# Kernel optimization log

Measured on AMD Instinct MI355X. Metric: run time of the kernel, lower is better.

The kernel has to match this reference:

```python
import jax, jax.numpy as jnp
import numpy as np

HEAD_DIM = 256
NUM_HEADS = 8
NUM_KV = 1
MAX_WAVELENGTH = 10000.0


def _apply_rope(x, positions):
    # x: [B, S, N, H], positions: [B, S] int
    d = x.shape[-1]
    freq_exponents = (2.0 / d) * jnp.arange(d // 2, dtype=jnp.float32)
    timescale = MAX_WAVELENGTH ** freq_exponents  # [H/2]
    radians = positions[..., None].astype(jnp.float32) / timescale  # [B, S, H/2]
    radians = radians[..., None, :]  # [B, S, 1, H/2]
    sin, cos = jnp.sin(radians), jnp.cos(radians)
    first, second = jnp.split(x.astype(jnp.float32), 2, axis=-1)
    out = jnp.concatenate([first * cos - second * sin, second * cos + first * sin], axis=-1)
    return out.astype(x.dtype)


def setup_inputs() -> dict:
    key = jax.random.key(0)
    ks = jax.random.split(key, 8)
    B, S0, S1 = 4, 768, 256
    W0, W1 = 2048, 1024
    T = S0 + S1
    s = 0.02  # param init scale
    x0 = jax.random.normal(ks[0], (B, S0, W0), jnp.float32)
    x1 = jax.random.normal(ks[1], (B, S1, W1), jnp.float32)
    w_q0 = jax.random.normal(ks[2], (NUM_HEADS, W0, HEAD_DIM), jnp.float32) * s
    w_kv0 = jax.random.normal(ks[3], (2, NUM_KV, W0, HEAD_DIM), jnp.float32) * s
    w_out0 = jax.random.normal(ks[4], (NUM_HEADS, HEAD_DIM, W0), jnp.float32) * s
    w_q1 = jax.random.normal(ks[5], (NUM_HEADS, W1, HEAD_DIM), jnp.float32) * s
    w_kv1 = jax.random.normal(ks[6], (2, NUM_KV, W1, HEAD_DIM), jnp.float32) * s
    w_out1 = jax.random.normal(ks[7], (NUM_HEADS, HEAD_DIM, W1), jnp.float32) * s
    positions = jnp.broadcast_to(jnp.arange(T, dtype=jnp.int32), (B, T))
    attn_mask = jnp.broadcast_to(jnp.tril(jnp.ones((T, T), bool))[None, None], (B, 1, T, T))
    return {"x0": x0, "x1": x1, "w_q0": w_q0, "w_kv0": w_kv0, "w_out0": w_out0,
            "w_q1": w_q1, "w_kv1": w_kv1, "w_out1": w_out1,
            "positions": positions, "attn_mask": attn_mask}


def reference(x0, x1, w_q0, w_kv0, w_out0, w_q1, w_kv1, w_out1, positions, attn_mask):
    dtype = x0.dtype
    # GQA projections per stream (num_kv_heads != num_heads path)
    q0 = jnp.einsum('BTD,NDH->BTNH', x0, w_q0)
    k0, v0 = jnp.einsum('BSD,CKDH->CBSKH', x0, w_kv0)
    q1 = jnp.einsum('BTD,NDH->BTNH', x1, w_q1)
    k1, v1 = jnp.einsum('BSD,CKDH->CBSKH', x1, w_kv1)
    q = jnp.concatenate([q0, q1], axis=1)  # [B, T, N, H]
    k = jnp.concatenate([k0, k1], axis=1)  # [B, T, K, H]
    v = jnp.concatenate([v0, v1], axis=1)
    q = _apply_rope(q, positions) * (HEAD_DIM ** -0.5)
    k = _apply_rope(k, positions)
    B, T = q.shape[0], q.shape[1]
    G = NUM_HEADS // NUM_KV
    q = q.reshape(B, T, NUM_KV, G, HEAD_DIM)
    logits = jnp.einsum('BTKGH,BSKH->BKGTS', q, k, preferred_element_type=jnp.float32)
    big_neg = -2.3819763e38
    masked = jnp.where(attn_mask[:, :, None, :, :], logits, big_neg)
    probs = jax.nn.softmax(masked, axis=-1).astype(dtype)
    encoded = jnp.einsum('BKGTS,BSKH->BTKGH', probs, v).reshape(B, T, NUM_HEADS, HEAD_DIM)
    S0 = x0.shape[1]
    out0 = jnp.einsum('BTNH,NHD->BTD', encoded[:, :S0], w_out0)
    out1 = jnp.einsum('BTNH,NHD->BTD', encoded[:, S0:], w_out1)
    return (out0, out1, k, v)
```

## Files before the change

kernel.cpp:

```cpp
#include <hip/hip_runtime.h>
#include <hip/hip_bf16.h>

typedef __attribute__((ext_vector_type(8))) short bf16x8;
typedef __attribute__((ext_vector_type(4))) float f32x4;
typedef __attribute__((ext_vector_type(4))) unsigned short u16x4;
typedef unsigned short US;

__device__ __forceinline__ f32x4 mfma16(bf16x8 a, bf16x8 b, f32x4 c) {
  return __builtin_amdgcn_mfma_f32_16x16x32_bf16(a, b, c, 0, 0, 0);
}

__device__ __forceinline__ US f2bf(float f) {
  union { float f; unsigned u; } x; x.f = f;
  unsigned r = x.u + 0x7fffu + ((x.u >> 16) & 1u);
  return (US)(r >> 16);
}

__device__ __forceinline__ void gld16(const US* gp, US* lp) {
  __builtin_amdgcn_global_load_lds(
      (const __attribute__((address_space(1))) unsigned*)gp,
      (__attribute__((address_space(3))) unsigned*)lp, 16, 0, 0);
}

__device__ __forceinline__ int permq(int h) {
  return ((h >> 5) << 6) + (h & 15) + (((h >> 4) & 1) << 5);
}

__device__ __forceinline__ int map_row(int r, int mode) {
  if (mode == 1) { int b = r / 768; return b * 1024 + (r - b * 768); }
  if (mode == 2) { int b = r >> 8; return b * 1024 + 768 + (r & 255); }
  return r;
}

__global__ __launch_bounds__(256)
void k_sincos(const int* __restrict__ pos, float2* __restrict__ sct) {
  int idx = blockIdx.x * 256 + threadIdx.x;
  int bt = idx >> 7, j = idx & 127;
  float inv_ts = powf(10000.0f, -(float)j * (1.0f / 128.0f));
  float r = (float)pos[bt] * inv_ts;
  sct[idx] = make_float2(sinf(r), cosf(r));
}

__global__ __launch_bounds__(256)
void k_prep(const float* __restrict__ x0, const float* __restrict__ x1,
            US* __restrict__ x0b, US* __restrict__ x1b,
            const float* __restrict__ wq0, const float* __restrict__ wkv0,
            const float* __restrict__ wq1, const float* __restrict__ wkv1,
            const float* __restrict__ wo0, const float* __restrict__ wo1,
            US* __restrict__ btq0, US* __restrict__ btkv0,
            US* __restrict__ btq1, US* __restrict__ btkv1,
            US* __restrict__ bto0, US* __restrict__ bto1) {
  const int bid = blockIdx.x;
  const int tid = threadIdx.x;
  if (bid < 7168) {
    const float* src; US* dst; int i;
    if (bid < 6144) { src = x0; dst = x0b; i = bid * 256 + tid; }
    else            { src = x1; dst = x1b; i = (bid - 6144) * 256 + tid; }
    f32x4 v = *reinterpret_cast<const f32x4*>(src + (size_t)i * 4);
    u16x4 o;
    o[0] = f2bf(v[0]); o[1] = f2bf(v[1]); o[2] = f2bf(v[2]); o[3] = f2bf(v[3]);
    *reinterpret_cast<u16x4*>(dst + (size_t)i * 4) = o;
    return;
  }
  __shared__ float tile[32][33];
  const float* src; US* dst; int R, C, CX, local; long sbs, dbs; bool pq = false;
  if (bid < 11264)      { local = bid - 7168;  src = wq0;  dst = btq0;  R = 2048; C = 256;  CX = 8;  sbs = 2048L * 256; dbs = 256L * 2048; pq = true; }
  else if (bid < 12288) { local = bid - 11264; src = wkv0; dst = btkv0; R = 2048; C = 256;  CX = 8;  sbs = 2048L * 256; dbs = 256L * 2048; }
  else if (bid < 14336) { local = bid - 12288; src = wq1;  dst = btq1;  R = 1024; C = 256;  CX = 8;  sbs = 1024L * 256; dbs = 256L * 1024; pq = true; }
  else if (bid < 14848) { local = bid - 14336; src = wkv1; dst = btkv1; R = 1024; C = 256;  CX = 8;  sbs = 1024L * 256; dbs = 256L * 1024; }
  else if (bid < 18944) { local = bid - 14848; src = wo0;  dst = bto0;  R = 2048; C = 2048; CX = 64; sbs = 0; dbs = 0; }
  else                  { local = bid - 18944; src = wo1;  dst = bto1;  R = 2048; C = 1024; CX = 32; sbs = 0; dbs = 0; }
  const int RY = R >> 5;
  const int cx = local % CX;
  const int rest = local / CX;
  const int ry = rest % RY;
  const int z = rest / RY;
  const int c0 = cx * 32, r0 = ry * 32;
  const int tx = tid & 31, ty = tid >> 5;
  src += (long)z * sbs;
  dst += (long)z * dbs;
#pragma unroll
  for (int i = 0; i < 4; ++i)
    tile[ty + 8 * i][tx] = src[(size_t)(r0 + ty + 8 * i) * C + c0 + tx];
  __syncthreads();
#pragma unroll
  for (int i = 0; i < 4; ++i) {
    int h = c0 + ty + 8 * i;
    int ph = pq ? ((h < 128) ? permq(h) : permq(h - 128) + 16) : h;
    dst[(size_t)ph * R + r0 + tx] = f2bf(tile[tx][ty + 8 * i]);
  }
}

template <int CMAP>
__global__ __launch_bounds__(256, 2)
void k_gemm_qkv(const US* __restrict__ A, const US* __restrict__ BT,
                US* __restrict__ q_bf, float* __restrict__ Ckv,
                const float2* __restrict__ sct, int M, int K) {
  __shared__ __align__(16) US lA[2][128 * 32];
  __shared__ __align__(16) US lB[2][128 * 32];
  const int tid = threadIdx.x;
  const int lane = tid & 63;
  const int wid = tid >> 6;
  const int wm = wid >> 1, wn = wid & 1;
  const int m0 = blockIdx.y * 128, n0 = blockIdx.x * 128;
  const int g = lane >> 4, c = lane & 15;
  const int lrow = lane >> 2, lcol = (lane & 3) * 8;
  const size_t ga0 = (size_t)(m0 + wid * 16 + lrow) * K + lcol;
  const size_t ga1 = (size_t)(m0 + 64 + wid * 16 + lrow) * K + lcol;
  const size_t gb0 = (size_t)(n0 + wid * 16 + lrow) * K + lcol;
  const size_t gb1 = (size_t)(n0 + 64 + wid * 16 + lrow) * K + lcol;

  auto stage = [&](int bi, int k0) {
    gld16(A + ga0 + k0, &lA[bi][(wid * 16) * 32]);
    gld16(A + ga1 + k0, &lA[bi][(64 + wid * 16) * 32]);
    gld16(BT + gb0 + k0, &lB[bi][(wid * 16) * 32]);
    gld16(BT + gb1 + k0, &lB[bi][(64 + wid * 16) * 32]);
  };

  f32x4 acc[4][4];
#pragma unroll
  for (int i = 0; i < 4; ++i)
#pragma unroll
    for (int j = 0; j < 4; ++j) acc[i][j] = f32x4{0.f, 0.f, 0.f, 0.f};

  const int nt = K >> 5;
  stage(0, 0);
  __syncthreads();
  for (int t = 0; t < nt; ++t) {
    const int bi = t & 1;
    if (t + 1 < nt) stage(bi ^ 1, (t + 1) * 32);
    bf16x8 af[4], bfr[4];
#pragma unroll
    for (int i = 0; i < 4; ++i) {
      af[i] = *reinterpret_cast<const bf16x8*>(&lA[bi][(wm * 64 + i * 16 + c) * 32 + g * 8]);
      bfr[i] = *reinterpret_cast<const bf16x8*>(&lB[bi][(wn * 64 + i * 16 + c) * 32 + g * 8]);
    }
#pragma unroll
    for (int i = 0; i < 4; ++i)
#pragma unroll
      for (int j = 0; j < 4; ++j)
        acc[i][j] = mfma16(af[i], bfr[j], acc[i][j]);
    __syncthreads();
  }

  const int colb = n0 + wn * 64;
  if (colb < 2048) {
    const int n = colb >> 8;
    const int base64 = colb & 255;
    const int h0 = (base64 >> 6) * 32 + c;
    const float scale = 0.0625f;
#pragma unroll
    for (int i = 0; i < 4; ++i) {
#pragma unroll
      for (int r = 0; r < 4; ++r) {
        const int orow = map_row(m0 + wm * 64 + i * 16 + 4 * g + r, CMAP);
        const float2 sc0 = sct[orow * 128 + h0];
        const float2 sc1 = sct[orow * 128 + h0 + 16];
        US* qp = q_bf + ((size_t)orow * 8 + n) * 256 + base64 + c;
        const float q1 = acc[i][0][r], q2 = acc[i][1][r];
        const float q3 = acc[i][2][r], q4 = acc[i][3][r];
        qp[0]  = f2bf(scale * (q1 * sc0.y - q2 * sc0.x));
        qp[16] = f2bf(scale * (q2 * sc0.y + q1 * sc0.x));
        qp[32] = f2bf(scale * (q3 * sc1.y - q4 * sc1.x));
        qp[48] = f2bf(scale * (q4 * sc1.y + q3 * sc1.x));
      }
    }
  } else {
    const int nb = colb - 2048 + c;
#pragma unroll
    for (int i = 0; i < 4; ++i) {
#pragma unroll
      for (int r = 0; r < 4; ++r) {
        const int orow = map_row(m0 + wm * 64 + i * 16 + 4 * g + r, CMAP);
        float* cp = Ckv + (size_t)orow * 512 + nb;
#pragma unroll
        for (int j = 0; j < 4; ++j) cp[j * 16] = acc[i][j][r];
      }
    }
  }
}

__global__ __launch_bounds__(256, 2)
void k_gemm_out(const US* __restrict__ A, const US* __restrict__ BT0, const US* __restrict__ BT1,
                float* __restrict__ C0, float* __restrict__ C1) {
  const int m0 = blockIdx.y * 128, n0 = blockIdx.x * 128;
  const int s0 = m0 & 1023;
  const bool is0 = (s0 < 768);
  if (!is0 && n0 >= 1024) return;
  const US* __restrict__ BT = is0 ? BT0 : BT1;
  const int K = 2048;
  __shared__ __align__(16) US lA[2][128 * 32];
  __shared__ __align__(16) US lB[2][128 * 32];
  const int tid = threadIdx.x;
  const int lane = tid & 63;
  const int wid = tid >> 6;
  const int wm = wid >> 1, wn = wid & 1;
  const int g = lane >> 4, c = lane & 15;
  const int lrow = lane >> 2, lcol = (lane & 3) * 8;
  const size_t ga0 = (size_t)(m0 + wid * 16 + lrow) * K + lcol;
  const size_t ga1 = (size_t)(m0 + 64 + wid * 16 + lrow) * K + lcol;
  const size_t gb0 = (size_t)(n0 + wid * 16 + lrow) * K + lcol;
  const size_t gb1 = (size_t)(n0 + 64 + wid * 16 + lrow) * K + lcol;

  auto stage = [&](int bi, int k0) {
    gld16(A + ga0 + k0, &lA[bi][(wid * 16) * 32]);
    gld16(A + ga1 + k0, &lA[bi][(64 + wid * 16) * 32]);
    gld16(BT + gb0 + k0, &lB[bi][(wid * 16) * 32]);
    gld16(BT + gb1 + k0, &lB[bi][(64 + wid * 16) * 32]);
  };

  f32x4 acc[4][4];
#pragma unroll
  for (int i = 0; i < 4; ++i)
#pragma unroll
    for (int j = 0; j < 4; ++j) acc[i][j] = f32x4{0.f, 0.f, 0.f, 0.f};

  const int nt = K >> 5;
  stage(0, 0);
  __syncthreads();
  for (int t = 0; t < nt; ++t) {
    const int bi = t & 1;
    if (t + 1 < nt) stage(bi ^ 1, (t + 1) * 32);
    bf16x8 af[4], bfr[4];
#pragma unroll
    for (int i = 0; i < 4; ++i) {
      af[i] = *reinterpret_cast<const bf16x8*>(&lA[bi][(wm * 64 + i * 16 + c) * 32 + g * 8]);
      bfr[i] = *reinterpret_cast<const bf16x8*>(&lB[bi][(wn * 64 + i * 16 + c) * 32 + g * 8]);
    }
#pragma unroll
    for (int i = 0; i < 4; ++i)
#pragma unroll
      for (int j = 0; j < 4; ++j)
        acc[i][j] = mfma16(af[i], bfr[j], acc[i][j]);
    __syncthreads();
  }

  const int col = n0 + wn * 64 + c;
#pragma unroll
  for (int i = 0; i < 4; ++i) {
#pragma unroll
    for (int r = 0; r < 4; ++r) {
      const int rf = m0 + wm * 64 + i * 16 + 4 * g + r;
      const int b = rf >> 10, s = rf & 1023;
      float* cp = is0 ? (C0 + (size_t)(b * 768 + s) * 2048 + col)
                      : (C1 + (size_t)(b * 256 + s - 768) * 1024 + col);
#pragma unroll
      for (int j = 0; j < 4; ++j) cp[j * 16] = acc[i][j][r];
    }
  }
}

__global__ __launch_bounds__(128)
void k_ropek(const float* __restrict__ kv_raw, const float2* __restrict__ sct,
             US* __restrict__ k_bf, float* __restrict__ k_out) {
  const int bt = blockIdx.x;
  const int j = threadIdx.x;
  const size_t ko = (size_t)bt * 512;
  const float x1 = kv_raw[ko + j], x2 = kv_raw[ko + j + 128];
  const float2 sc = sct[bt * 128 + j];
  const float o1 = x1 * sc.y - x2 * sc.x, o2 = x2 * sc.y + x1 * sc.x;
  const size_t kd = (size_t)bt * 256;
  const int p = permq(j);
  k_bf[kd + p] = f2bf(o1);
  k_bf[kd + p + 16] = f2bf(o2);
  k_out[kd + j] = o1;
  k_out[kd + j + 128] = o2;
}

__global__ __launch_bounds__(256)
void k_vtrans(const float* __restrict__ kv_raw, float* __restrict__ v_out, US* __restrict__ vt) {
  __shared__ float tile[32][33];
  int t0 = blockIdx.x * 32, h0 = blockIdx.y * 32, b = blockIdx.z;
  int tx = threadIdx.x, ty = threadIdx.y;
#pragma unroll
  for (int i = 0; i < 4; ++i) {
    int t = t0 + ty + 8 * i;
    float v = kv_raw[(size_t)(b * 1024 + t) * 512 + 256 + h0 + tx];
    tile[ty + 8 * i][tx] = v;
    v_out[(size_t)(b * 1024 + t) * 256 + h0 + tx] = v;
  }
  __syncthreads();
#pragma unroll
  for (int i = 0; i < 4; ++i) {
    int h = h0 + ty + 8 * i;
    vt[(size_t)(b * 256 + h) * 1024 + t0 + tx] = f2bf(tile[tx][ty + 8 * i]);
  }
}

__global__ __launch_bounds__(256, 2)
void k_attn(const US* __restrict__ qb, const US* __restrict__ kb,
            const US* __restrict__ vt, US* __restrict__ enc) {
  __shared__ __align__(16) US lK[2][32 * 256];
  __shared__ __align__(16) US lV[2][256 * 32];
  const int id = blockIdx.x;
  const int r0_ = (id < 256) ? id : 767 - id;
  const int qt = 63 - (r0_ >> 3);
  const int hg = (r0_ >> 2) & 1;
  const int b = r0_ & 3;
  const int tid = threadIdx.x;
  const int wid = tid >> 6;
  const int lane = tid & 63;
  const int g = lane >> 4, c = lane & 15;
  const int qbase = qt * 16;
  const int n = hg * 4 + wid;

  const US* kbB = kb + (size_t)b * 262144;
  const US* vtB = vt + (size_t)b * 262144;

  bf16x8 qf[8];
  {
    const US* qp = qb + ((size_t)((b * 1024 + qbase + c) * 8 + n)) * 256 + 8 * g;
#pragma unroll
    for (int ch = 0; ch < 8; ++ch)
      qf[ch] = *reinterpret_cast<const bf16x8*>(qp + ch * 32);
  }

  auto stage = [&](int bi, int c0) {
#pragma unroll
    for (int j = 0; j < 4; ++j) {
      const int rk = wid * 8 + j * 2 + (lane >> 5);
      const int sk = lane & 31;
      gld16(kbB + (size_t)(c0 + rk) * 256 + (sk ^ (rk & 7)) * 8,
            &lK[bi][(wid * 8 + j * 2) * 256]);
      const int rv = wid * 64 + j * 16 + (lane >> 2);
      const int sv = lane & 3;
      gld16(vtB + (size_t)rv * 1024 + c0 + (sv ^ ((rv >> 1) & 3)) * 8,
            &lV[bi][(wid * 64 + j * 16) * 32]);
    }
  };

  f32x4 acc[16];
#pragma unroll
  for (int i = 0; i < 16; ++i) acc[i] = f32x4{0.f, 0.f, 0.f, 0.f};
  float m_run = -3.0e38f, l_run = 0.f;

  const int nC = qbase / 32 + 1;
  stage(0, 0);
  __syncthreads();

  for (int i = 0; i < nC; ++i) {
    const int c0 = 32 * i;
    const int bi = i & 1;
    if (i + 1 < nC) stage(bi ^ 1, c0 + 32);

    const bool hb = (c0 + 16 <= qbase);
    f32x4 sA = {0.f, 0.f, 0.f, 0.f}, sB = {0.f, 0.f, 0.f, 0.f};
    __builtin_amdgcn_s_setprio(1);
#pragma unroll
    for (int ch = 0; ch < 8; ++ch) {
      const int slot = (((ch * 4 + g) ^ (c & 7)) * 8);
      sA = mfma16(*reinterpret_cast<const bf16x8*>(&lK[bi][c * 256 + slot]), qf[ch], sA);
    }
    if (hb) {
#pragma unroll
      for (int ch = 0; ch < 8; ++ch) {
        const int slot = (((ch * 4 + g) ^ (c & 7)) * 8);
        sB = mfma16(*reinterpret_cast<const bf16x8*>(&lK[bi][(c + 16) * 256 + slot]), qf[ch], sB);
      }
    }
    __builtin_amdgcn_s_setprio(0);
    if (c0 == qbase) {
#pragma unroll
      for (int r = 0; r < 4; ++r)
        if (4 * g + r > c) sA[r] = -3.0e38f;
    }
    if (hb && (c0 + 16 == qbase)) {
#pragma unroll
      for (int r = 0; r < 4; ++r)
        if (4 * g + r > c) sB[r] = -3.0e38f;
    }
    float tm = fmaxf(fmaxf(sA[0], sA[1]), fmaxf(sA[2], sA[3]));
    if (hb) tm = fmaxf(tm, fmaxf(fmaxf(sB[0], sB[1]), fmaxf(sB[2], sB[3])));
    tm = fmaxf(tm, __shfl_xor(tm, 16));
    tm = fmaxf(tm, __shfl_xor(tm, 32));
    if (!__all(tm - m_run <= 8.0f)) {
      const float m_new = fmaxf(m_run, tm);
      const float alpha = __expf(m_run - m_new);
      float aacc[4];
#pragma unroll
      for (int r = 0; r < 4; ++r) aacc[r] = __shfl(alpha, 4 * g + r);
#pragma unroll
      for (int ht = 0; ht < 16; ++ht) {
        acc[ht][0] *= aacc[0]; acc[ht][1] *= aacc[1];
        acc[ht][2] *= aacc[2]; acc[ht][3] *= aacc[3];
      }
      l_run *= alpha;
      m_run = m_new;
    }
    float pA[4], pB[4];
    float ls = 0.f;
#pragma unroll
    for (int r = 0; r < 4; ++r) { pA[r] = __expf(sA[r] - m_run); ls += pA[r]; }
#pragma unroll
    for (int r = 0; r < 4; ++r) { pB[r] = hb ? __expf(sB[r] - m_run) : 0.f; ls += pB[r]; }
    ls += __shfl_xor(ls, 16);
    ls += __shfl_xor(ls, 32);
    l_run += ls;
    bf16x8 paf;
#pragma unroll
    for (int j = 0; j < 8; ++j) {
      const int srcl = ((2 * (g & 1) + (j >> 2)) << 4) + c;
      float va = __shfl(pA[j & 3], srcl);
      float vb = __shfl(pB[j & 3], srcl);
      float pv = (g < 2) ? va : vb;
      paf[j] = (short)f2bf(pv);
    }
    __builtin_amdgcn_s_setprio(1);
#pragma unroll
    for (int ht = 0; ht < 16; ++ht) {
      const int h = ht * 16 + c;
      const int slot = (g ^ ((c >> 1) & 3)) * 8;
      bf16x8 vf = *reinterpret_cast<const bf16x8*>(&lV[bi][h * 32 + slot]);
      acc[ht] = mfma16(paf, vf, acc[ht]);
    }
    __builtin_amdgcn_s_setprio(0);
    __syncthreads();
  }

  const float inv = 1.0f / l_run;
  float ia[4];
#pragma unroll
  for (int r = 0; r < 4; ++r) ia[r] = __shfl(inv, 4 * g + r);
#pragma unroll
  for (int ht = 0; ht < 16; ++ht) {
#pragma unroll
    for (int r = 0; r < 4; ++r) {
      size_t o = ((size_t)((b * 1024 + qbase + 4 * g + r) * 8 + n)) * 256 + ht * 16 + c;
      enc[o] = f2bf(acc[ht][r] * ia[r]);
    }
  }
}

extern "C" void kernel_launch(void* const* d_in, const int* in_sizes, int n_in,
                              void* d_out, int out_size, void* d_ws, size_t ws_size,
                              hipStream_t stream) {
  const float* x0 = (const float*)d_in[0];
  const float* x1 = (const float*)d_in[1];
  const float* wq0 = (const float*)d_in[2];
  const float* wkv0 = (const float*)d_in[3];
  const float* wo0 = (const float*)d_in[4];
  const float* wq1 = (const float*)d_in[5];
  const float* wkv1 = (const float*)d_in[6];
  const float* wo1 = (const float*)d_in[7];
  const int* pos = (const int*)d_in[8];
  float* out = (float*)d_out;

  float* out0 = out;
  float* out1 = out + 6291456;
  float* k_out = out + 7340032;
  float* v_out = out + 8388608;

  char* ws = (char*)d_ws;
  size_t off = 0;
  auto alloc = [&](size_t bytes) {
    char* p = ws + off;
    off += (bytes + 255) & ~(size_t)255;
    return p;
  };
  US* x0b   = (US*)alloc(6291456ull * 2);
  US* x1b   = (US*)alloc(1048576ull * 2);
  US* btq0  = (US*)alloc(2048ull * 2048 * 2);
  US* btkv0 = (US*)alloc(512ull * 2048 * 2);
  US* btq1  = (US*)alloc(2048ull * 1024 * 2);
  US* btkv1 = (US*)alloc(512ull * 1024 * 2);
  US* bto0  = (US*)alloc(2048ull * 2048 * 2);
  US* bto1  = (US*)alloc(1024ull * 2048 * 2);
  float* kv_raw = (float*)alloc(2097152ull * 4);
  US* q_bf = (US*)alloc(8388608ull * 2);
  US* k_bf = (US*)alloc(1048576ull * 2);
  US* vt   = (US*)alloc(1048576ull * 2 + 256);
  US* enc  = (US*)alloc(8388608ull * 2);
  float2* sct = (float2*)alloc(524288ull * 8);

  k_sincos<<<2048, 256, 0, stream>>>(pos, sct);

  k_prep<<<20992, 256, 0, stream>>>(x0, x1, x0b, x1b, wq0, wkv0, wq1, wkv1, wo0, wo1,
                                    btq0, btkv0, btq1, btkv1, bto0, bto1);

  k_gemm_qkv<1><<<dim3(20, 24), 256, 0, stream>>>(x0b, btq0, q_bf, kv_raw, sct, 3072, 2048);
  k_gemm_qkv<2><<<dim3(20, 8), 256, 0, stream>>>(x1b, btq1, q_bf, kv_raw, sct, 1024, 1024);

  k_ropek<<<4096, 128, 0, stream>>>(kv_raw, sct, k_bf, k_out);
  k_vtrans<<<dim3(32, 8, 4), dim3(32, 8), 0, stream>>>(kv_raw, v_out, vt);

  k_attn<<<512, 256, 0, stream>>>(q_bf, k_bf, vt, enc);

  k_gemm_out<<<dim3(16, 32), 256, 0, stream>>>(enc, bto0, bto1, out0, out1);
}
```

Before: 215.4 us.

## Merge small launches into fewer kernels and compact GEMM grids with XCD swizzle

Folds the sin/cos table into the prep kernel, merges the two QKV GEMM launches into one flat grid, and merges K-rope with the V transpose. The output GEMM grid is compacted so no blocks exit early, and block ids are remapped so consecutive tiles are spread across the eight XCDs. The goal is to cut launch overhead and idle tail blocks. It adds runtime branching on cmap instead of a template constant, which may cost a little in address math.

```diff
diff --git a/kernel.cpp b/kernel.cpp
--- a/kernel.cpp
+++ b/kernel.cpp
@@ -30,15 +30,6 @@
   if (mode == 1) { int b = r / 768; return b * 1024 + (r - b * 768); }
   if (mode == 2) { int b = r >> 8; return b * 1024 + 768 + (r & 255); }
   return r;
-}
-
-__global__ __launch_bounds__(256)
-void k_sincos(const int* __restrict__ pos, float2* __restrict__ sct) {
-  int idx = blockIdx.x * 256 + threadIdx.x;
-  int bt = idx >> 7, j = idx & 127;
-  float inv_ts = powf(10000.0f, -(float)j * (1.0f / 128.0f));
-  float r = (float)pos[bt] * inv_ts;
-  sct[idx] = make_float2(sinf(r), cosf(r));
 }
 
 __global__ __launch_bounds__(256)
@@ -49,9 +40,18 @@
             const float* __restrict__ wo0, const float* __restrict__ wo1,
             US* __restrict__ btq0, US* __restrict__ btkv0,
             US* __restrict__ btq1, US* __restrict__ btkv1,
-            US* __restrict__ bto0, US* __restrict__ bto1) {
+            US* __restrict__ bto0, US* __restrict__ bto1,
+            const int* __restrict__ pos, float2* __restrict__ sct) {
   const int bid = blockIdx.x;
   const int tid = threadIdx.x;
+  if (bid >= 20992) {
+    int idx = (bid - 20992) * 256 + tid;
+    int bt = idx >> 7, j = idx & 127;
+    float inv_ts = powf(10000.0f, -(float)j * (1.0f / 128.0f));
+    float r = (float)pos[bt] * inv_ts;
+    sct[idx] = make_float2(sinf(r), cosf(r));
+    return;
+  }
   if (bid < 7168) {
     const float* src; US* dst; int i;
     if (bid < 6144) { src = x0; dst = x0b; i = bid * 256 + tid; }
@@ -91,18 +91,24 @@
   }
 }
 
-template <int CMAP>
 __global__ __launch_bounds__(256, 2)
-void k_gemm_qkv(const US* __restrict__ A, const US* __restrict__ BT,
+void k_gemm_qkv(const US* __restrict__ x0b, const US* __restrict__ x1b,
+                const US* __restrict__ btq0, const US* __restrict__ btq1,
                 US* __restrict__ q_bf, float* __restrict__ Ckv,
-                const float2* __restrict__ sct, int M, int K) {
+                const float2* __restrict__ sct) {
+  const int bid = blockIdx.x;
+  int id = (bid & 7) * 80 + (bid >> 3);
+  const US* A; const US* BT; int K, cmap, by, bx;
+  if (id < 480) { A = x0b; BT = btq0; K = 2048; cmap = 1; by = id / 20; bx = id % 20; }
+  else { id -= 480; A = x1b; BT = btq1; K = 1024; cmap = 2; by = id / 20; bx = id % 20; }
+
   __shared__ __align__(16) US lA[2][128 * 32];
   __shared__ __align__(16) US lB[2][128 * 32];
   const int tid = threadIdx.x;
   const int lane = tid & 63;
   const int wid = tid >> 6;
   const int wm = wid >> 1, wn = wid & 1;
-  const int m0 = blockIdx.y * 128, n0 = blockIdx.x * 128;
+  const int m0 = by * 128, n0 = bx * 128;
   const int g = lane >> 4, c = lane & 15;
   const int lrow = lane >> 2, lcol = (lane & 3) * 8;
   const size_t ga0 = (size_t)(m0 + wid * 16 + lrow) * K + lcol;
@@ -153,7 +159,7 @@
     for (int i = 0; i < 4; ++i) {
 #pragma unroll
       for (int r = 0; r < 4; ++r) {
-        const int orow = map_row(m0 + wm * 64 + i * 16 + 4 * g + r, CMAP);
+        const int orow = map_row(m0 + wm * 64 + i * 16 + 4 * g + r, cmap);
         const float2 sc0 = sct[orow * 128 + h0];
         const float2 sc1 = sct[orow * 128 + h0 + 16];
         US* qp = q_bf + ((size_t)orow * 8 + n) * 256 + base64 + c;
@@ -171,7 +177,7 @@
     for (int i = 0; i < 4; ++i) {
 #pragma unroll
       for (int r = 0; r < 4; ++r) {
-        const int orow = map_row(m0 + wm * 64 + i * 16 + 4 * g + r, CMAP);
+        const int orow = map_row(m0 + wm * 64 + i * 16 + 4 * g + r, cmap);
         float* cp = Ckv + (size_t)orow * 512 + nb;
 #pragma unroll
         for (int j = 0; j < 4; ++j) cp[j * 16] = acc[i][j][r];
@@ -183,11 +189,12 @@
 __global__ __launch_bounds__(256, 2)
 void k_gemm_out(const US* __restrict__ A, const US* __restrict__ BT0, const US* __restrict__ BT1,
                 float* __restrict__ C0, float* __restrict__ C1) {
-  const int m0 = blockIdx.y * 128, n0 = blockIdx.x * 128;
-  const int s0 = m0 & 1023;
-  const bool is0 = (s0 < 768);
-  if (!is0 && n0 >= 1024) return;
-  const US* __restrict__ BT = is0 ? BT0 : BT1;
+  const int bid = blockIdx.x;
+  int id = (bid & 7) * 56 + (bid >> 3);
+  const US* BT; float* Cb; int amap, mt, ntile, Nst;
+  if (id < 384) { amap = 1; mt = id / 16; ntile = id % 16; BT = BT0; Cb = C0; Nst = 2048; }
+  else { id -= 384; amap = 2; mt = id / 8; ntile = id % 8; BT = BT1; Cb = C1; Nst = 1024; }
+  const int m0 = mt * 128, n0 = ntile * 128;
   const int K = 2048;
   __shared__ __align__(16) US lA[2][128 * 32];
   __shared__ __align__(16) US lB[2][128 * 32];
@@ -197,8 +204,8 @@
   const int wm = wid >> 1, wn = wid & 1;
   const int g = lane >> 4, c = lane & 15;
   const int lrow = lane >> 2, lcol = (lane & 3) * 8;
-  const size_t ga0 = (size_t)(m0 + wid * 16 + lrow) * K + lcol;
-  const size_t ga1 = (size_t)(m0 + 64 + wid * 16 + lrow) * K + lcol;
+  const size_t ga0 = (size_t)map_row(m0 + wid * 16 + lrow, amap) * K + lcol;
+  const size_t ga1 = (size_t)map_row(m0 + 64 + wid * 16 + lrow, amap) * K + lcol;
   const size_t gb0 = (size_t)(n0 + wid * 16 + lrow) * K + lcol;
   const size_t gb1 = (size_t)(n0 + 64 + wid * 16 + lrow) * K + lcol;
 
@@ -240,38 +247,38 @@
   for (int i = 0; i < 4; ++i) {
 #pragma unroll
     for (int r = 0; r < 4; ++r) {
-      const int rf = m0 + wm * 64 + i * 16 + 4 * g + r;
-      const int b = rf >> 10, s = rf & 1023;
-      float* cp = is0 ? (C0 + (size_t)(b * 768 + s) * 2048 + col)
-                      : (C1 + (size_t)(b * 256 + s - 768) * 1024 + col);
+      const int orow = m0 + wm * 64 + i * 16 + 4 * g + r;
+      float* cp = Cb + (size_t)orow * Nst + col;
 #pragma unroll
       for (int j = 0; j < 4; ++j) cp[j * 16] = acc[i][j][r];
     }
   }
 }
 
-__global__ __launch_bounds__(128)
-void k_ropek(const float* __restrict__ kv_raw, const float2* __restrict__ sct,
-             US* __restrict__ k_bf, float* __restrict__ k_out) {
-  const int bt = blockIdx.x;
-  const int j = threadIdx.x;
-  const size_t ko = (size_t)bt * 512;
-  const float x1 = kv_raw[ko + j], x2 = kv_raw[ko + j + 128];
-  const float2 sc = sct[bt * 128 + j];
-  const float o1 = x1 * sc.y - x2 * sc.x, o2 = x2 * sc.y + x1 * sc.x;
-  const size_t kd = (size_t)bt * 256;
-  const int p = permq(j);
-  k_bf[kd + p] = f2bf(o1);
-  k_bf[kd + p + 16] = f2bf(o2);
-  k_out[kd + j] = o1;
-  k_out[kd + j + 128] = o2;
-}
-
 __global__ __launch_bounds__(256)
-void k_vtrans(const float* __restrict__ kv_raw, float* __restrict__ v_out, US* __restrict__ vt) {
+void k_postkv(const float* __restrict__ kv_raw, const float2* __restrict__ sct,
+              US* __restrict__ k_bf, float* __restrict__ k_out,
+              float* __restrict__ v_out, US* __restrict__ vt) {
+  const int bid = blockIdx.x;
+  const int tid = threadIdx.x;
+  if (bid >= 1024) {
+    const int bt = (bid - 1024) * 2 + (tid >> 7);
+    const int j = tid & 127;
+    const size_t ko = (size_t)bt * 512;
+    const float x1 = kv_raw[ko + j], x2 = kv_raw[ko + j + 128];
+    const float2 sc = sct[bt * 128 + j];
+    const float o1 = x1 * sc.y - x2 * sc.x, o2 = x2 * sc.y + x1 * sc.x;
+    const size_t kd = (size_t)bt * 256;
+    const int p = permq(j);
+    k_bf[kd + p] = f2bf(o1);
+    k_bf[kd + p + 16] = f2bf(o2);
+    k_out[kd + j] = o1;
+    k_out[kd + j + 128] = o2;
+    return;
+  }
   __shared__ float tile[32][33];
-  int t0 = blockIdx.x * 32, h0 = blockIdx.y * 32, b = blockIdx.z;
-  int tx = threadIdx.x, ty = threadIdx.y;
+  const int t0 = (bid & 31) * 32, h0 = ((bid >> 5) & 7) * 32, b = bid >> 8;
+  const int tx = tid & 31, ty = tid >> 5;
 #pragma unroll
   for (int i = 0; i < 4; ++i) {
     int t = t0 + ty + 8 * i;
@@ -471,19 +478,16 @@
   US* vt   = (US*)alloc(1048576ull * 2 + 256);
   US* enc  = (US*)alloc(8388608ull * 2);
   float2* sct = (float2*)alloc(524288ull * 8);
-
-  k_sincos<<<2048, 256, 0, stream>>>(pos, sct);
-
-  k_prep<<<20992, 256, 0, stream>>>(x0, x1, x0b, x1b, wq0, wkv0, wq1, wkv1, wo0, wo1,
-                                    btq0, btkv0, btq1, btkv1, bto0, bto1);
-
-  k_gemm_qkv<1><<<dim3(20, 24), 256, 0, stream>>>(x0b, btq0, q_bf, kv_raw, sct, 3072, 2048);
-  k_gemm_qkv<2><<<dim3(20, 8), 256, 0, stream>>>(x1b, btq1, q_bf, kv_raw, sct, 1024, 1024);
-
-  k_ropek<<<4096, 128, 0, stream>>>(kv_raw, sct, k_bf, k_out);
-  k_vtrans<<<dim3(32, 8, 4), dim3(32, 8), 0, stream>>>(kv_raw, v_out, vt);
+  (void)btkv0; (void)btkv1;
+
+  k_prep<<<23040, 256, 0, stream>>>(x0, x1, x0b, x1b, wq0, wkv0, wq1, wkv1, wo0, wo1,
+                                    btq0, btkv0, btq1, btkv1, bto0, bto1, pos, sct);
+
+  k_gemm_qkv<<<640, 256, 0, stream>>>(x0b, x1b, btq0, btq1, q_bf, kv_raw, sct);
+
+  k_postkv<<<3072, 256, 0, stream>>>(kv_raw, sct, k_bf, k_out, v_out, vt);
 
   k_attn<<<512, 256, 0, stream>>>(q_bf, k_bf, vt, enc);
 
-  k_gemm_out<<<dim3(16, 32), 256, 0, stream>>>(enc, bto0, bto1, out0, out1);
-}
+  k_gemm_out<<<448, 256, 0, stream>>>(enc, bto0, bto1, out0, out1);
+}
```

Result: faster. 199.1 us (-7.6%).
